# Performance work log

Measured on AMD Instinct MI355X. Metric: run time of the kernel, lower is better.

## Reference

```python
import jax, jax.numpy as jnp
import numpy as np

DIM = 512
HEADS = 8
DIM_HEAD = 64
SCALE = DIM_HEAD ** -0.5


def setup_inputs() -> dict:
    key = jax.random.key(0)
    k1, k2, k3, k4, k5 = jax.random.split(key, 5)
    inner = HEADS * DIM_HEAD
    x = jax.random.normal(k1, (16, DIM, 32, 32), dtype=jnp.float32)
    W_proj = jax.random.normal(k2, (DIM, inner * 3), dtype=jnp.float32) * (DIM ** -0.5)
    b_proj = jax.random.normal(k3, (inner * 3,), dtype=jnp.float32) * 0.01
    W_out = jax.random.normal(k4, (inner, DIM), dtype=jnp.float32) * (inner ** -0.5)
    b_out = jax.random.normal(k5, (DIM,), dtype=jnp.float32) * 0.01
    return {"x": x, "W_proj": W_proj, "b_proj": b_proj, "W_out": W_out, "b_out": b_out}


def reference(x, W_proj, b_proj, W_out, b_out):
    b, c, hh, ww = x.shape
    s = hh * ww
    xs = x.reshape(b, c, s).transpose(0, 2, 1)  # b s c
    qkv = xs @ W_proj + b_proj                  # b s (heads * 3*dim_head)
    qkv = qkv.reshape(b, s, HEADS, 3 * DIM_HEAD)
    q, k, v = jnp.split(qkv, 3, axis=-1)        # each: b s h d
    w = jnp.einsum('bshd,bthd->bsth', q, k) * SCALE
    w = jax.nn.softmax(w, axis=2)
    res = jnp.einsum('bsth,bthd->bshd', w, v).reshape(b, s, HEADS * DIM_HEAD)
    out = res @ W_out + b_out + xs              # b s c (residual)
    return out.transpose(0, 2, 1).reshape(b, c, hh, ww)
```

## Files before the change

kernel.cpp:

```cpp
#include <hip/hip_runtime.h>
#include <hip/hip_bf16.h>

#define BATCH 16
#define CDIM  512
#define SEQ   1024
#define HEADS 8
#define DHEAD 64
#define N3    1536
#define QSCALE 0.18033688011112042f

typedef unsigned short ushort_t;
typedef __attribute__((ext_vector_type(8))) short short8;
typedef __attribute__((ext_vector_type(4))) float f32x4;

__device__ __forceinline__ unsigned f2bf(float f) {
    unsigned u = __float_as_uint(f);
    u += 0x7fffu + ((u >> 16) & 1u);
    return u >> 16;
}
__device__ __forceinline__ float fast_exp2(float x) {
    float r;
    asm("v_exp_f32 %0, %1" : "=v"(r) : "v"(x));
    return r;
}
__device__ __forceinline__ unsigned pack_bf16_trunc(float lo, float hi) {
    return __builtin_amdgcn_perm(__float_as_uint(hi), __float_as_uint(lo), 0x07060302u);
}
__device__ __forceinline__ void async16(const void* g, void* l) {
    __builtin_amdgcn_global_load_lds(
        (const __attribute__((address_space(1))) unsigned int*)g,
        (__attribute__((address_space(3))) unsigned int*)l, 16, 0, 0);
}
__device__ __forceinline__ void barrier_raw() {
    __builtin_amdgcn_sched_barrier(0);
    __builtin_amdgcn_s_barrier();
    __builtin_amdgcn_sched_barrier(0);
}
#define WAIT_VMCNT(n) asm volatile("s_waitcnt vmcnt(" #n ")" ::: "memory")


__global__ __launch_bounds__(256) void blockify_kernel(
    const float* __restrict__ x, const float* __restrict__ Wp,
    const float* __restrict__ Wo,
    ushort_t* __restrict__ xtb, ushort_t* __restrict__ WpTb,
    ushort_t* __restrict__ WoTb)
{
    const int zz = blockIdx.z;
    const float* in;
    ushort_t* out;
    int C, zbat;
    if (zz < 16)       { if (blockIdx.x >= 16) return; in = x;  out = xtb;  C = 1024; zbat = zz; }
    else if (zz == 16) {                               in = Wp; out = WpTb; C = 1536; zbat = 0;  }
    else               { if (blockIdx.x >= 8)  return; in = Wo; out = WoTb; C = 512;  zbat = 0;  }

    __shared__ float t[64][68];
    const int k0 = blockIdx.y * 64, c0 = blockIdx.x * 64;
    const float* inb = in + (size_t)zbat * 512 * C;
    const int tid = threadIdx.x;
#pragma unroll
    for (int i = 0; i < 4; ++i) {
        int idx = tid + i * 256;
        int r = idx >> 4, c4 = idx & 15;
        float4 f = *(const float4*)&inb[(size_t)(k0 + r) * C + c0 + c4 * 4];
        *(float4*)&t[r][c4 * 4] = f;
    }
    __syncthreads();
    const size_t mbase = (size_t)zbat * C + c0;
    const int ml = tid & 63;
#pragma unroll
    for (int i = 0; i < 2; ++i) {
        int oct = (tid >> 6) + i * 4;
        size_t m = mbase + ml;
        int mt = (int)(m >> 7), mr = (int)(m & 127);
        int m16 = mr >> 4, col = mr & 15;
        int k = k0 + oct * 8;
        int it = k >> 5, q = (k >> 3) & 3;
        uint4 pk;
        pk.x = f2bf(t[oct * 8 + 0][ml]) | (f2bf(t[oct * 8 + 1][ml]) << 16);
        pk.y = f2bf(t[oct * 8 + 2][ml]) | (f2bf(t[oct * 8 + 3][ml]) << 16);
        pk.z = f2bf(t[oct * 8 + 4][ml]) | (f2bf(t[oct * 8 + 5][ml]) << 16);
        pk.w = f2bf(t[oct * 8 + 6][ml]) | (f2bf(t[oct * 8 + 7][ml]) << 16);
        size_t off = ((size_t)(mt * 16 + it) * 8 + m16) * 512 + (q * 16 + col) * 8;
        *(uint4*)&out[off] = pk;
    }
}

__global__ __launch_bounds__(256) void qkv_gemm_kernel(
    const ushort_t* __restrict__ xtb, const ushort_t* __restrict__ WpTb,
    const float* __restrict__ bp,
    ushort_t* __restrict__ q_buf, ushort_t* __restrict__ kb,
    ushort_t* __restrict__ vb)
{
    __shared__ alignas(16) ushort_t Asub[2][8 * 512];
    __shared__ alignas(16) ushort_t Bsub[2][8 * 512];

    const int tid = threadIdx.x, w = tid >> 6, lane = tid & 63;
    const int quad = lane >> 4, col = lane & 15;
    const int wm = w >> 1, wn = w & 1;

    const int lin = blockIdx.x + 12 * blockIdx.y;
    const int xcd = lin & 7;
    const int rr  = lin >> 3;
    const int n0  = (rr % 12) * 128;
    const int m0  = ((rr / 12) * 8 + xcd) * 128;

    f32x4 acc[4][4];
#pragma unroll
    for (int i = 0; i < 4; ++i)
#pragma unroll
        for (int j = 0; j < 4; ++j) acc[i][j] = (f32x4){0.f, 0.f, 0.f, 0.f};

    const ushort_t* Ab = xtb  + (size_t)(m0 >> 7) * 65536 + (w * 2) * 512 + lane * 8;
    const ushort_t* Bb = WpTb + (size_t)(n0 >> 7) * 65536 + (w * 2) * 512 + lane * 8;

#define QKV_STAGE(buf, t)                                         \
    do {                                                          \
        async16(Ab + (t) * 4096,       &Asub[buf][(w * 2 + 0) * 512]); \
        async16(Ab + (t) * 4096 + 512, &Asub[buf][(w * 2 + 1) * 512]); \
        async16(Bb + (t) * 4096,       &Bsub[buf][(w * 2 + 0) * 512]); \
        async16(Bb + (t) * 4096 + 512, &Bsub[buf][(w * 2 + 1) * 512]); \
    } while (0)

    QKV_STAGE(0, 0);
    QKV_STAGE(1, 1);
    for (int it = 0; it < 16; ++it) {
        const int cur = it & 1;
        if (it < 15) { WAIT_VMCNT(4); } else { WAIT_VMCNT(0); }
        barrier_raw();

        short8 af[4], bfr[4];
#pragma unroll
        for (int i = 0; i < 4; ++i) af[i]  = *(const short8*)&Asub[cur][(wm * 4 + i) * 512 + lane * 8];
#pragma unroll
        for (int j = 0; j < 4; ++j) bfr[j] = *(const short8*)&Bsub[cur][(wn * 4 + j) * 512 + lane * 8];
#pragma unroll
        for (int i = 0; i < 4; ++i)
#pragma unroll
            for (int j = 0; j < 4; ++j)
                acc[i][j] = __builtin_amdgcn_mfma_f32_16x16x32_bf16(af[i], bfr[j], acc[i][j], 0, 0, 0);

        if (it < 14) {
            barrier_raw();
            QKV_STAGE(cur, it + 2);
        }
    }
#undef QKV_STAGE

    const int b = m0 >> 10, s0 = m0 & 1023;
    const size_t b8 = (size_t)b * HEADS;
#pragma unroll
    for (int j = 0; j < 4; ++j) {
        int nb = n0 + wn * 64 + j * 16;
        int h = nb / 192, rem = nb % 192;
        int type = rem >> 6, dbase = rem & 63;
        float bias = bp[nb + col];
        size_t bh = b8 + h;
        int d = dbase + col;
#pragma unroll
        for (int i = 0; i < 4; ++i) {
            int sb = s0 + wm * 64 + i * 16 + quad * 4;
            f32x4 v = acc[i][j];
            if (type == 2) {
                unsigned lo = f2bf(v[0] + bias) | (f2bf(v[1] + bias) << 16);
                unsigned hi = f2bf(v[2] + bias) | (f2bf(v[3] + bias) << 16);
                uint2 pk; pk.x = lo; pk.y = hi;
                int itv = sb >> 6, sub = (d >> 4) * 2 + ((sb >> 5) & 1);
                size_t off = ((bh * 16 + itv) * 8 + sub) * 512
                           + (((sb >> 2) & 3) * 16 + (d & 15)) * 8
                           + ((sb >> 4) & 1) * 4;
                *(uint2*)&vb[off] = pk;
            } else if (type == 1) {
#pragma unroll
                for (int r = 0; r < 4; ++r) {
                    int t = sb + r;
                    int itk = t >> 6, sub = ((t >> 4) & 3) * 2 + (d >> 5);
                    size_t off = ((bh * 16 + itk) * 8 + sub) * 512
                               + (((d >> 3) & 3) * 16 + (t & 15)) * 8 + (d & 7);
                    kb[off] = (ushort_t)f2bf(v[r] + bias);
                }
            } else {
#pragma unroll
                for (int r = 0; r < 4; ++r)
                    q_buf[(bh * SEQ + sb + r) * DHEAD + d] =
                        (ushort_t)f2bf((v[r] + bias) * QSCALE);
            }
        }
    }
}

__global__ __launch_bounds__(128) void attn_kernel(
    const ushort_t* __restrict__ q_buf, const ushort_t* __restrict__ kb,
    const ushort_t* __restrict__ vb, ushort_t* __restrict__ resb)
{
    __shared__ alignas(16) ushort_t Kf[2][8 * 512];

    const int tid  = threadIdx.x;
    const int w    = tid >> 6;
    const int lane = tid & 63;
    const int quad = lane >> 4;
    const int col  = lane & 15;

    const int bhid = blockIdx.x;
    const int b = bhid >> 3, h = bhid & 7;
    const int q0 = blockIdx.y * 128;
    const size_t bh = (size_t)b * HEADS + h;

    const ushort_t* qp = q_buf + ((bh * SEQ) + q0 + w * 64 + col) * DHEAD + quad * 8;
    short8 qf0[4], qf1[4];
#pragma unroll
    for (int g = 0; g < 4; ++g) {
        qf0[g] = *(const short8*)(qp + g * 16 * DHEAD);
        qf1[g] = *(const short8*)(qp + g * 16 * DHEAD + 32);
    }

    short8 ones;
#pragma unroll
    for (int i = 0; i < 8; ++i) ones[i] = (short)0x3F80;

    f32x4 O[4][4];
#pragma unroll
    for (int g = 0; g < 4; ++g)
#pragma unroll
        for (int i = 0; i < 4; ++i) O[g][i] = (f32x4){0.f, 0.f, 0.f, 0.f};
    f32x4 L[4];
#pragma unroll
    for (int g = 0; g < 4; ++g) L[g] = (f32x4){0.f, 0.f, 0.f, 0.f};

    const ushort_t* kaB = kb + (size_t)bh * 65536 + (w * 4) * 512 + lane * 8;
    const ushort_t* vgB = vb + (size_t)bh * 65536 + lane * 8;

#define ATTN_STAGE(buf)                                            \
    do {                                                           \
        async16(kaB,        &Kf[buf][(w * 4 + 0) * 512]);          \
        async16(kaB + 512,  &Kf[buf][(w * 4 + 1) * 512]);          \
        async16(kaB + 1024, &Kf[buf][(w * 4 + 2) * 512]);          \
        async16(kaB + 1536, &Kf[buf][(w * 4 + 3) * 512]);          \
        kaB += 4096;                                               \
    } while (0)

    ATTN_STAGE(0);

    for (int it = 0; it < 16; ++it) {
        const int cur = it & 1;
        const ushort_t* kc = Kf[cur];
        __syncthreads();

        short8 vf[8];
#pragma unroll
        for (int i = 0; i < 8; ++i)
            vf[i] = *(const short8*)&vgB[(size_t)it * 4096 + i * 512];

        if (it < 15) ATTN_STAGE(cur ^ 1);

        short8 kf[8];
#pragma unroll
        for (int t16 = 0; t16 < 4; ++t16) {
            kf[2 * t16 + 0] = *(const short8*)&kc[(t16 * 2 + 0) * 512 + lane * 8];
            kf[2 * t16 + 1] = *(const short8*)&kc[(t16 * 2 + 1) * 512 + lane * 8];
        }

        short8 pf[4][2];
#pragma unroll
        for (int g = 0; g < 4; ++g) {
            f32x4 S[4];
            __builtin_amdgcn_s_setprio(1);
#pragma unroll
            for (int t16 = 0; t16 < 4; ++t16) {
                f32x4 a = (f32x4){0.f, 0.f, 0.f, 0.f};
                a = __builtin_amdgcn_mfma_f32_16x16x32_bf16(kf[2 * t16 + 0], qf0[g], a, 0, 0, 0);
                a = __builtin_amdgcn_mfma_f32_16x16x32_bf16(kf[2 * t16 + 1], qf1[g], a, 0, 0, 0);
                S[t16] = a;
            }
            __builtin_amdgcn_s_setprio(0);
            union { uint4 u; short8 s; } p0, p1;
            p0.u.x = pack_bf16_trunc(fast_exp2(S[0][0]), fast_exp2(S[0][1]));
            p0.u.y = pack_bf16_trunc(fast_exp2(S[0][2]), fast_exp2(S[0][3]));
            p0.u.z = pack_bf16_trunc(fast_exp2(S[1][0]), fast_exp2(S[1][1]));
            p0.u.w = pack_bf16_trunc(fast_exp2(S[1][2]), fast_exp2(S[1][3]));
            p1.u.x = pack_bf16_trunc(fast_exp2(S[2][0]), fast_exp2(S[2][1]));
            p1.u.y = pack_bf16_trunc(fast_exp2(S[2][2]), fast_exp2(S[2][3]));
            p1.u.z = pack_bf16_trunc(fast_exp2(S[3][0]), fast_exp2(S[3][1]));
            p1.u.w = pack_bf16_trunc(fast_exp2(S[3][2]), fast_exp2(S[3][3]));
            pf[g][0] = p0.s;
            pf[g][1] = p1.s;
        }

#pragma unroll
        for (int d16 = 0; d16 < 4; ++d16) {
            const short8 v0 = vf[d16 * 2 + 0];
            const short8 v1 = vf[d16 * 2 + 1];
            __builtin_amdgcn_s_setprio(1);
#pragma unroll
            for (int g = 0; g < 4; ++g) {
                O[g][d16] = __builtin_amdgcn_mfma_f32_16x16x32_bf16(pf[g][0], v0, O[g][d16], 0, 0, 0);
                O[g][d16] = __builtin_amdgcn_mfma_f32_16x16x32_bf16(pf[g][1], v1, O[g][d16], 0, 0, 0);
            }
            __builtin_amdgcn_s_setprio(0);
        }
#pragma unroll
        for (int g = 0; g < 4; ++g) {
            L[g] = __builtin_amdgcn_mfma_f32_16x16x32_bf16(pf[g][0], ones, L[g], 0, 0, 0);
            L[g] = __builtin_amdgcn_mfma_f32_16x16x32_bf16(pf[g][1], ones, L[g], 0, 0, 0);
        }
    }
#undef ATTN_STAGE

    const int mt = b * 8 + (q0 >> 7);
#pragma unroll
    for (int g = 0; g < 4; ++g) {
        const int m16 = w * 4 + g;
#pragma unroll
        for (int r = 0; r < 4; ++r) {
            float inv = 1.f / L[g][r];
            const int mcol = quad * 4 + r;
#pragma unroll
            for (int d16 = 0; d16 < 4; ++d16) {
                int itk = h * 2 + (d16 >> 1);
                int kq = (d16 & 1) * 2 + (col >> 3);
                size_t off = ((size_t)(mt * 16 + itk) * 8 + m16) * 512
                           + (kq * 16 + mcol) * 8 + (col & 7);
                resb[off] = (ushort_t)f2bf(O[g][d16][r] * inv);
            }
        }
    }
}

__global__ __launch_bounds__(256) void out_gemm_kernel(
    const ushort_t* __restrict__ resb, const ushort_t* __restrict__ WoTb,
    const float* __restrict__ bo, const float* __restrict__ x,
    float* __restrict__ out)
{
    __shared__ alignas(16) ushort_t SMEM[(2 * 4 + 2 * 8) * 512];
    ushort_t (*Asub)[4 * 512] = (ushort_t (*)[4 * 512])(SMEM);
    ushort_t (*Bsub)[8 * 512] = (ushort_t (*)[8 * 512])(SMEM + 2 * 4 * 512);
    float* tb = (float*)SMEM;

    const int tid = threadIdx.x, w = tid >> 6, lane = tid & 63;
    const int quad = lane >> 4, col = lane & 15;
    const int wm = w >> 1, wn = w & 1;

    const int lin = blockIdx.x + 4 * blockIdx.y;
    const int xcd = lin & 7;
    const int rr  = lin >> 3;
    const int n0  = (rr & 3) * 128;
    const int m0  = ((rr >> 2) * 8 + xcd) * 64;

    f32x4 acc[2][4];
#pragma unroll
    for (int i = 0; i < 2; ++i)
#pragma unroll
        for (int j = 0; j < 4; ++j) acc[i][j] = (f32x4){0.f, 0.f, 0.f, 0.f};

    const int mt = m0 >> 7, mhalf = (m0 >> 6) & 1;
    const ushort_t* Ab = resb + (size_t)mt * 65536 + (size_t)(mhalf * 4 + w) * 512 + lane * 8;
    const ushort_t* Bb = WoTb + (size_t)(n0 >> 7) * 65536 + (w * 2) * 512 + lane * 8;

#define OUT_STAGE(buf, t)                                              \
    do {                                                               \
        async16(Ab + (t) * 4096,       &Asub[buf][w * 512]);           \
        async16(Bb + (t) * 4096,       &Bsub[buf][(w * 2 + 0) * 512]); \
        async16(Bb + (t) * 4096 + 512, &Bsub[buf][(w * 2 + 1) * 512]); \
    } while (0)

    OUT_STAGE(0, 0);
    OUT_STAGE(1, 1);
    for (int it = 0; it < 16; ++it) {
        const int cur = it & 1;
        if (it < 15) { WAIT_VMCNT(3); } else { WAIT_VMCNT(0); }
        barrier_raw();

        short8 af[2], bfr[4];
#pragma unroll
        for (int i = 0; i < 2; ++i) af[i]  = *(const short8*)&Asub[cur][(wm * 2 + i) * 512 + lane * 8];
#pragma unroll
        for (int j = 0; j < 4; ++j) bfr[j] = *(const short8*)&Bsub[cur][(wn * 4 + j) * 512 + lane * 8];
#pragma unroll
        for (int i = 0; i < 2; ++i)
#pragma unroll
            for (int j = 0; j < 4; ++j)
                acc[i][j] = __builtin_amdgcn_mfma_f32_16x16x32_bf16(af[i], bfr[j], acc[i][j], 0, 0, 0);

        if (it < 14) {
            barrier_raw();
            OUT_STAGE(cur, it + 2);
        }
    }
#undef OUT_STAGE

    const int b = m0 >> 10, s0 = m0 & 1023;
#pragma unroll
    for (int j = 0; j < 4; ++j) {
        __syncthreads();
#pragma unroll
        for (int i = 0; i < 2; ++i) {
            f32x4 v = acc[i][j];
            float* dst = &tb[(wn * 16 + col) * 68 + wm * 32 + i * 16 + quad * 4];
            dst[0] = v[0]; dst[1] = v[1]; dst[2] = v[2]; dst[3] = v[3];
        }
        __syncthreads();
#pragma unroll
        for (int p = 0; p < 2; ++p) {
            int nl = w * 8 + p * 4 + (lane >> 4);
            int n = n0 + j * 16 + (nl & 15) + (nl >> 4) * 64;
            int scol = (lane & 15) * 4;
            float4 t4 = *(const float4*)&tb[nl * 68 + scol];
            size_t o = ((size_t)b * CDIM + n) * SEQ + s0 + scol;
            float4 xr = *(const float4*)&x[o];
            float bias = bo[n];
            float4 ov;
            ov.x = t4.x + bias + xr.x;
            ov.y = t4.y + bias + xr.y;
            ov.z = t4.z + bias + xr.z;
            ov.w = t4.w + bias + xr.w;
            *(float4*)&out[o] = ov;
        }
    }
}

extern "C" void kernel_launch(void* const* d_in, const int* in_sizes, int n_in,
                              void* d_out, int out_size, void* d_ws, size_t ws_size,
                              hipStream_t stream) {
    const float* x  = (const float*)d_in[0];
    const float* Wp = (const float*)d_in[1];
    const float* bp = (const float*)d_in[2];
    const float* Wo = (const float*)d_in[3];
    const float* bo = (const float*)d_in[4];
    float* out = (float*)d_out;

    ushort_t* xtb   = (ushort_t*)d_ws;
    ushort_t* WpTb  = xtb   + (size_t)8388608;
    ushort_t* WoTb  = WpTb  + (size_t)786432;
    ushort_t* q_buf = WoTb  + (size_t)262144;
    ushort_t* kb    = q_buf + (size_t)8388608;
    ushort_t* vb    = kb    + (size_t)8388608;
    ushort_t* resb  = vb    + (size_t)8388608;

    blockify_kernel<<<dim3(24, 8, 18), 256, 0, stream>>>(x, Wp, Wo, xtb, WpTb, WoTb);
    qkv_gemm_kernel<<<dim3(12, 128), 256, 0, stream>>>(xtb, WpTb, bp, q_buf, kb, vb);
    attn_kernel<<<dim3(128, 8), 128, 0, stream>>>(q_buf, kb, vb, resb);
    out_gemm_kernel<<<dim3(4, 256), 256, 0, stream>>>(resb, WoTb, bo, x, out);
}
```

Before: 187.1 us.

## Fuse x transpose and bf16 conversion into QKV GEMM A-tile loads

Removes the blockify pass over x that wrote a bf16 blocked copy to workspace, and has the QKV GEMM read fp32 x directly, converting and packing it into LDS itself. This drops a 16 MB write plus re-read of the transposed activations. In exchange the GEMM now issues 16 scalar 4-byte global loads per lane per stage instead of async LDS copies, does the conversion in registers and waits synchronously on LDS stores, and x is re-read by each of the 12 N-tiles in fp32.

```diff
diff --git a/kernel.cpp b/kernel.cpp
--- a/kernel.cpp
+++ b/kernel.cpp
@@ -37,41 +37,37 @@
     __builtin_amdgcn_sched_barrier(0);
 }
 #define WAIT_VMCNT(n) asm volatile("s_waitcnt vmcnt(" #n ")" ::: "memory")
+#define WAIT_LGKMCNT0() asm volatile("s_waitcnt lgkmcnt(0)" ::: "memory")
 
 
 __global__ __launch_bounds__(256) void blockify_kernel(
-    const float* __restrict__ x, const float* __restrict__ Wp,
-    const float* __restrict__ Wo,
-    ushort_t* __restrict__ xtb, ushort_t* __restrict__ WpTb,
-    ushort_t* __restrict__ WoTb)
+    const float* __restrict__ Wp, const float* __restrict__ Wo,
+    ushort_t* __restrict__ WpTb, ushort_t* __restrict__ WoTb)
 {
     const int zz = blockIdx.z;
     const float* in;
     ushort_t* out;
-    int C, zbat;
-    if (zz < 16)       { if (blockIdx.x >= 16) return; in = x;  out = xtb;  C = 1024; zbat = zz; }
-    else if (zz == 16) {                               in = Wp; out = WpTb; C = 1536; zbat = 0;  }
-    else               { if (blockIdx.x >= 8)  return; in = Wo; out = WoTb; C = 512;  zbat = 0;  }
+    int C;
+    if (zz == 0) {                              in = Wp; out = WpTb; C = 1536; }
+    else         { if (blockIdx.x >= 8) return; in = Wo; out = WoTb; C = 512;  }
 
     __shared__ float t[64][68];
     const int k0 = blockIdx.y * 64, c0 = blockIdx.x * 64;
-    const float* inb = in + (size_t)zbat * 512 * C;
     const int tid = threadIdx.x;
 #pragma unroll
     for (int i = 0; i < 4; ++i) {
         int idx = tid + i * 256;
         int r = idx >> 4, c4 = idx & 15;
-        float4 f = *(const float4*)&inb[(size_t)(k0 + r) * C + c0 + c4 * 4];
+        float4 f = *(const float4*)&in[(size_t)(k0 + r) * C + c0 + c4 * 4];
         *(float4*)&t[r][c4 * 4] = f;
     }
     __syncthreads();
-    const size_t mbase = (size_t)zbat * C + c0;
     const int ml = tid & 63;
 #pragma unroll
     for (int i = 0; i < 2; ++i) {
         int oct = (tid >> 6) + i * 4;
-        size_t m = mbase + ml;
-        int mt = (int)(m >> 7), mr = (int)(m & 127);
+        int m = c0 + ml;
+        int mt = m >> 7, mr = m & 127;
         int m16 = mr >> 4, col = mr & 15;
         int k = k0 + oct * 8;
         int it = k >> 5, q = (k >> 3) & 3;
@@ -86,7 +82,7 @@
 }
 
 __global__ __launch_bounds__(256) void qkv_gemm_kernel(
-    const ushort_t* __restrict__ xtb, const ushort_t* __restrict__ WpTb,
+    const float* __restrict__ x, const ushort_t* __restrict__ WpTb,
     const float* __restrict__ bp,
     ushort_t* __restrict__ q_buf, ushort_t* __restrict__ kb,
     ushort_t* __restrict__ vb)
@@ -104,28 +100,45 @@
     const int n0  = (rr % 12) * 128;
     const int m0  = ((rr / 12) * 8 + xcd) * 128;
 
+    const int b = m0 >> 10, s0 = m0 & 1023;
+    const float* xb = x + (size_t)b * 512 * 1024;
+
     f32x4 acc[4][4];
 #pragma unroll
     for (int i = 0; i < 4; ++i)
 #pragma unroll
         for (int j = 0; j < 4; ++j) acc[i][j] = (f32x4){0.f, 0.f, 0.f, 0.f};
 
-    const ushort_t* Ab = xtb  + (size_t)(m0 >> 7) * 65536 + (w * 2) * 512 + lane * 8;
     const ushort_t* Bb = WpTb + (size_t)(n0 >> 7) * 65536 + (w * 2) * 512 + lane * 8;
 
-#define QKV_STAGE(buf, t)                                         \
-    do {                                                          \
-        async16(Ab + (t) * 4096,       &Asub[buf][(w * 2 + 0) * 512]); \
-        async16(Ab + (t) * 4096 + 512, &Asub[buf][(w * 2 + 1) * 512]); \
-        async16(Bb + (t) * 4096,       &Bsub[buf][(w * 2 + 0) * 512]); \
-        async16(Bb + (t) * 4096 + 512, &Bsub[buf][(w * 2 + 1) * 512]); \
+#define QKV_STAGE(buf, t)                                                    \
+    do {                                                                     \
+        float va[2][8];                                                      \
+        _Pragma("unroll")                                                    \
+        for (int mm = 0; mm < 2; ++mm)                                       \
+            _Pragma("unroll")                                                \
+            for (int jj = 0; jj < 8; ++jj)                                   \
+                va[mm][jj] = xb[(size_t)((t) * 32 + quad * 8 + jj) * 1024    \
+                                + s0 + (w * 2 + mm) * 16 + col];             \
+        async16(Bb + (t) * 4096,       &Bsub[buf][(w * 2 + 0) * 512]);       \
+        async16(Bb + (t) * 4096 + 512, &Bsub[buf][(w * 2 + 1) * 512]);       \
+        _Pragma("unroll")                                                    \
+        for (int mm = 0; mm < 2; ++mm) {                                     \
+            uint4 pk;                                                        \
+            pk.x = f2bf(va[mm][0]) | (f2bf(va[mm][1]) << 16);                \
+            pk.y = f2bf(va[mm][2]) | (f2bf(va[mm][3]) << 16);                \
+            pk.z = f2bf(va[mm][4]) | (f2bf(va[mm][5]) << 16);                \
+            pk.w = f2bf(va[mm][6]) | (f2bf(va[mm][7]) << 16);                \
+            *(uint4*)&Asub[buf][(w * 2 + mm) * 512 + lane * 8] = pk;         \
+        }                                                                    \
     } while (0)
 
     QKV_STAGE(0, 0);
     QKV_STAGE(1, 1);
     for (int it = 0; it < 16; ++it) {
         const int cur = it & 1;
-        if (it < 15) { WAIT_VMCNT(4); } else { WAIT_VMCNT(0); }
+        if (it < 15) { WAIT_VMCNT(2); } else { WAIT_VMCNT(0); }
+        WAIT_LGKMCNT0();
         barrier_raw();
 
         short8 af[4], bfr[4];
@@ -146,7 +159,6 @@
     }
 #undef QKV_STAGE
 
-    const int b = m0 >> 10, s0 = m0 & 1023;
     const size_t b8 = (size_t)b * HEADS;
 #pragma unroll
     for (int j = 0; j < 4; ++j) {
@@ -427,16 +439,15 @@
     const float* bo = (const float*)d_in[4];
     float* out = (float*)d_out;
 
-    ushort_t* xtb   = (ushort_t*)d_ws;
-    ushort_t* WpTb  = xtb   + (size_t)8388608;
+    ushort_t* WpTb  = (ushort_t*)d_ws;
     ushort_t* WoTb  = WpTb  + (size_t)786432;
     ushort_t* q_buf = WoTb  + (size_t)262144;
     ushort_t* kb    = q_buf + (size_t)8388608;
     ushort_t* vb    = kb    + (size_t)8388608;
     ushort_t* resb  = vb    + (size_t)8388608;
 
-    blockify_kernel<<<dim3(24, 8, 18), 256, 0, stream>>>(x, Wp, Wo, xtb, WpTb, WoTb);
-    qkv_gemm_kernel<<<dim3(12, 128), 256, 0, stream>>>(xtb, WpTb, bp, q_buf, kb, vb);
+    blockify_kernel<<<dim3(24, 8, 2), 256, 0, stream>>>(Wp, Wo, WpTb, WoTb);
+    qkv_gemm_kernel<<<dim3(12, 128), 256, 0, stream>>>(x, WpTb, bp, q_buf, kb, vb);
     attn_kernel<<<dim3(128, 8), 128, 0, stream>>>(q_buf, kb, vb, resb);
     out_gemm_kernel<<<dim3(4, 256), 256, 0, stream>>>(resb, WoTb, bo, x, out);
 }
```

After: 207.0 us. +10.6%, slower.
